# Kernel tuning notes

Hardware: AMD Instinct MI355X
Metric: run time of the kernel (lower is better)

Reference implementation:

```python
import jax, jax.numpy as jnp
import numpy as np

B, S, H, F, G = 8, 2048, 1024, 4096, 128
EPS = 1e-5


def setup_inputs() -> dict:
    key = jax.random.key(0)
    ks = jax.random.split(key, 8)
    x = jax.random.normal(ks[0], (B, S, H), dtype=jnp.float32)
    ln_gamma = jnp.ones((H,), jnp.float32)
    ln_beta = jnp.zeros((H,), jnp.float32)
    # int8-style quantized weights stored as int32 in [0, 256) with zero-point 128
    fc1_q = jax.random.randint(ks[1], (H, F), 0, 256, dtype=jnp.int32)
    fc2_q = jax.random.randint(ks[2], (F, H), 0, 256, dtype=jnp.int32)
    # per-group scales (one scale per 128 rows of K, per output column)
    fc1_scales = jax.random.uniform(ks[3], (H // G, F), jnp.float32) * 0.02 + 0.001
    fc2_scales = jax.random.uniform(ks[4], (F // G, H), jnp.float32) * 0.02 + 0.001
    fc1_bias = jax.random.normal(ks[5], (F,), jnp.float32) * 0.02
    fc2_bias = jax.random.normal(ks[6], (H,), jnp.float32) * 0.02
    return {"x": x, "ln_gamma": ln_gamma, "ln_beta": ln_beta,
            "fc1_q": fc1_q, "fc1_scales": fc1_scales, "fc1_bias": fc1_bias,
            "fc2_q": fc2_q, "fc2_scales": fc2_scales, "fc2_bias": fc2_bias}


def _dequant(q, scales, g):
    # q: [K, N] int, scales: [K//g, N]; zero-point 128 symmetric int8 scheme
    K, N = q.shape
    w = (q.astype(jnp.float32) - 128.0).reshape(K // g, g, N) * scales[:, None, :]
    return w.reshape(K, N)


def reference(x, ln_gamma, ln_beta, fc1_q, fc1_scales, fc1_bias, fc2_q, fc2_scales, fc2_bias):
    residual = x
    # LayerNorm over last dim
    mu = jnp.mean(x, axis=-1, keepdims=True)
    var = jnp.mean(jnp.square(x - mu), axis=-1, keepdims=True)
    h = (x - mu) * jax.lax.rsqrt(var + EPS) * ln_gamma + ln_beta
    hf = h.reshape(-1, H)                       # [B*S, H]
    w1 = _dequant(fc1_q, fc1_scales, G)         # [H, F]
    y = hf @ w1 + fc1_bias                      # [B*S, F]
    y = jax.nn.silu(y)                          # dropout is identity at inference
    w2 = _dequant(fc2_q, fc2_scales, G)         # [F, H]
    z = y @ w2 + fc2_bias                       # [B*S, H]
    return residual + 0.5 * z.reshape(residual.shape)
```

## Files before the change

kernel.cpp:

```cpp
#include <hip/hip_runtime.h>
#include <hip/hip_bf16.h>

#define HH 1024
#define FF 4096
#define MTOT (8 * 2048)

typedef __attribute__((ext_vector_type(4))) float f32x4;
typedef __attribute__((ext_vector_type(8))) short bf16x8;

__device__ inline void async_load16(const void* g, void* l) {
    __builtin_amdgcn_global_load_lds(
        (const __attribute__((address_space(1))) unsigned int*)g,
        (__attribute__((address_space(3))) unsigned int*)l, 16, 0, 0);
}
__device__ inline unsigned lds_off(void* p) {
    return (unsigned)(size_t)(__attribute__((address_space(3))) char*)p;
}
template<int OFF>
__device__ inline bf16x8 dsr(unsigned addr) {
    bf16x8 r;
    asm volatile("ds_read_b128 %0, %1 offset:%2" : "=v"(r) : "v"(addr), "n"(OFF));
    return r;
}
#define SBAR()  __builtin_amdgcn_s_barrier()
template<int N>
__device__ inline void LGKM() {
    asm volatile("s_waitcnt lgkmcnt(%0)" :: "n"(N));
    __builtin_amdgcn_sched_barrier(0);
}
#define WAIT_VM0() asm volatile("s_waitcnt vmcnt(0)")

template<int BUF, int MH>
__device__ inline void ldA(bf16x8 (&d)[4][2], unsigned vA0, unsigned vA1) {
    constexpr int B = BUF * 32768 + MH * 8192;
    d[0][0] = dsr<B + 0>(vA0);     d[0][1] = dsr<B + 0>(vA1);
    d[1][0] = dsr<B + 2048>(vA0);  d[1][1] = dsr<B + 2048>(vA1);
    d[2][0] = dsr<B + 4096>(vA0);  d[2][1] = dsr<B + 4096>(vA1);
    d[3][0] = dsr<B + 6144>(vA0);  d[3][1] = dsr<B + 6144>(vA1);
}
template<int BUF, int NH>
__device__ inline void ldB(bf16x8 (&d)[2][2], unsigned vB0, unsigned vB1) {
    constexpr int B = BUF * 32768 + NH * 4096;
    d[0][0] = dsr<B + 0>(vB0);     d[0][1] = dsr<B + 0>(vB1);
    d[1][0] = dsr<B + 2048>(vB0);  d[1][1] = dsr<B + 2048>(vB1);
}

__global__ void dequant_t_kernel(const int* __restrict__ q,
                                 const float* __restrict__ scales,
                                 __hip_bfloat16* __restrict__ wt,
                                 int K, int N)
{
    __shared__ float tile[32][33];
    const int n0 = blockIdx.x * 32, k0 = blockIdx.y * 32;
    const int tx = threadIdx.x, ty = threadIdx.y;
#pragma unroll
    for (int i = 0; i < 32; i += 8) {
        int k = k0 + ty + i, n = n0 + tx;
        float s = scales[(size_t)(k >> 7) * N + n];
        tile[ty + i][tx] = (float)(q[(size_t)k * N + n] - 128) * s;
    }
    __syncthreads();
#pragma unroll
    for (int i = 0; i < 32; i += 8) {
        int n = n0 + ty + i, k = k0 + tx;
        wt[(size_t)n * K + k] = __float2bfloat16(tile[tx][ty + i]);
    }
}

__global__ __launch_bounds__(256)
void ln_kernel(const float* __restrict__ x, const float* __restrict__ gamma,
               const float* __restrict__ beta, __hip_bfloat16* __restrict__ hf,
               int m0)
{
    const int row = m0 + blockIdx.x;
    const float4 v = ((const float4*)(x + (size_t)row * HH))[threadIdx.x];
    float s  = v.x + v.y + v.z + v.w;
    float ss = v.x * v.x + v.y * v.y + v.z * v.z + v.w * v.w;
#pragma unroll
    for (int o = 32; o > 0; o >>= 1) { s += __shfl_down(s, o); ss += __shfl_down(ss, o); }
    __shared__ float red[8];
    const int wid = threadIdx.x >> 6, lane = threadIdx.x & 63;
    if (lane == 0) { red[wid] = s; red[4 + wid] = ss; }
    __syncthreads();
    if (threadIdx.x == 0) {
        red[0] = red[0] + red[1] + red[2] + red[3];
        red[4] = red[4] + red[5] + red[6] + red[7];
    }
    __syncthreads();
    const float mu   = red[0] * (1.f / HH);
    const float rstd = rsqrtf(red[4] * (1.f / HH) - mu * mu + 1e-5f);
    const float4 g = ((const float4*)gamma)[threadIdx.x];
    const float4 b = ((const float4*)beta)[threadIdx.x];
    float h0 = (v.x - mu) * rstd * g.x + b.x;
    float h1 = (v.y - mu) * rstd * g.y + b.y;
    float h2 = (v.z - mu) * rstd * g.z + b.z;
    float h3 = (v.w - mu) * rstd * g.w + b.w;
    __hip_bfloat16 t0 = __float2bfloat16(h0), t1 = __float2bfloat16(h1);
    __hip_bfloat16 t2 = __float2bfloat16(h2), t3 = __float2bfloat16(h3);
    ushort4 o;
    o.x = *(unsigned short*)&t0; o.y = *(unsigned short*)&t1;
    o.z = *(unsigned short*)&t2; o.w = *(unsigned short*)&t3;
    ((ushort4*)(hf + (size_t)blockIdx.x * HH))[threadIdx.x] = o;
}

template<int EPI, int KK>
__global__ __launch_bounds__(512, 2)
void gemm256(const __hip_bfloat16* __restrict__ A,
             const __hip_bfloat16* __restrict__ Bt,
             const float* __restrict__ bias,
             const float* __restrict__ resid,
             void* __restrict__ outv,
             int N, int nbx)
{
    __shared__ __align__(16) short SM[65536];
    constexpr int NT = KK >> 6;

    const int nwg = (int)gridDim.x, b = (int)blockIdx.x;
    const int q = nwg >> 3, r = nwg & 7;
    const int xcd = b & 7, pos = b >> 3;
    const int bid = (xcd < r) ? xcd * (q + 1) + pos
                              : r * (q + 1) + (xcd - r) * q + pos;
    const int bx = bid % nbx, by = bid / nbx;
    const int rowA0 = by * 256, colB0 = bx * 256;

    const int tid = (int)threadIdx.x;
    const int lane = tid & 63, wid = tid >> 6;
    const int wr = wid >> 2, wc = wid & 3;
    const int lrow = lane & 15, kg = lane >> 4;
    const int swz = lrow & 7;

    const int srow = tid >> 3;
    const int sgs  = (tid & 7) ^ (srow & 7);
    const __hip_bfloat16* aSrc = A  + (size_t)(rowA0 + srow) * KK + sgs * 8;
    const __hip_bfloat16* bSrc = Bt + (size_t)(colB0 + srow) * KK + sgs * 8;
    short* aDst = SM + srow * 64 + (tid & 7) * 8;
    short* bDst = SM + 32768 + srow * 64 + (tid & 7) * 8;

    const unsigned asB = lds_off(SM);
    const unsigned k0off = (unsigned)((kg ^ swz) << 4);
    const unsigned k1off = (unsigned)(((4 + kg) ^ swz) << 4);
    const unsigned vA0 = asB + (unsigned)((wr * 128 + lrow) * 128) + k0off;
    const unsigned vA1 = asB + (unsigned)((wr * 128 + lrow) * 128) + k1off;
    const unsigned vB0 = asB + 65536u + (unsigned)((wc * 64 + lrow) * 128) + k0off;
    const unsigned vB1 = asB + 65536u + (unsigned)((wc * 64 + lrow) * 128) + k1off;

    auto stA = [&](int buf, int t, int half) {
        const size_t ko = (size_t)t * 64;
        short* d = aDst + buf * 16384 + half * 8192;
        const __hip_bfloat16* s0 = aSrc + (size_t)(half * 128) * KK + ko;
        async_load16(s0, d);
        async_load16(s0 + (size_t)64 * KK, d + 4096);
    };
    auto stB = [&](int buf, int t, int half) {
        const size_t ko = (size_t)t * 64;
        short* d = bDst + buf * 16384 + half * 8192;
        const __hip_bfloat16* s0 = bSrc + (size_t)(half * 128) * KK + ko;
        async_load16(s0, d);
        async_load16(s0 + (size_t)64 * KK, d + 4096);
    };

    f32x4 acc[8][4] = {};
    auto mf = [&](const bf16x8 (&a)[4][2], const bf16x8 (&bb)[2][2], int mh, int nh) {
        __builtin_amdgcn_s_setprio(1);
#pragma unroll
        for (int ks = 0; ks < 2; ++ks)
#pragma unroll
            for (int m2 = 0; m2 < 4; ++m2)
#pragma unroll
                for (int n2 = 0; n2 < 2; ++n2)
                    acc[mh * 4 + m2][nh * 2 + n2] =
                        __builtin_amdgcn_mfma_f32_16x16x32_bf16(
                            a[m2][ks], bb[n2][ks], acc[mh * 4 + m2][nh * 2 + n2], 0, 0, 0);
        __builtin_amdgcn_s_setprio(0);
    };

    stA(0, 0, 0); stA(0, 0, 1); stB(0, 0, 0); stB(0, 0, 1);
    WAIT_VM0();
    SBAR();

    bf16x8 a0[4][2], a1[4][2], b0[2][2], b1[2][2];
    const int NI = NT >> 1;
    for (int i = 0; i < NI; ++i) {
        const int c = 2 * i, n = 2 * i + 1;
        stA(1, n, 0); stA(1, n, 1); stB(1, n, 0); stB(1, n, 1);
        ldA<0, 0>(a0, vA0, vA1);
        ldB<0, 0>(b0, vB0, vB1);
        ldB<0, 1>(b1, vB0, vB1);
        ldA<0, 1>(a1, vA0, vA1);
        LGKM<12>();
        mf(a0, b0, 0, 0);
        LGKM<8>();
        mf(a0, b1, 0, 1);
        LGKM<0>();
        mf(a1, b0, 1, 0);
        mf(a1, b1, 1, 1);
        WAIT_VM0();
        SBAR();
        if (i < NI - 1) { stA(0, c + 2, 0); stA(0, c + 2, 1);
                          stB(0, c + 2, 0); stB(0, c + 2, 1); }
        ldA<1, 0>(a0, vA0, vA1);
        ldB<1, 0>(b0, vB0, vB1);
        ldB<1, 1>(b1, vB0, vB1);
        ldA<1, 1>(a1, vA0, vA1);
        LGKM<12>();
        mf(a0, b0, 0, 0);
        LGKM<8>();
        mf(a0, b1, 0, 1);
        LGKM<0>();
        mf(a1, b0, 1, 0);
        mf(a1, b1, 1, 1);
        WAIT_VM0();
        SBAR();
    }

    __syncthreads();

    if (EPI == 0) {
        short* smh = SM;
#pragma unroll
        for (int ni = 0; ni < 4; ++ni) {
            const int col = wc * 64 + ni * 16 + lrow;
            const float bv = bias[colB0 + col];
#pragma unroll
            for (int mi = 0; mi < 8; ++mi) {
#pragma unroll
                for (int j = 0; j < 4; ++j) {
                    const int rowl = wr * 128 + mi * 16 + kg * 4 + j;
                    const float v = acc[mi][ni][j] + bv;
                    const float sv = v / (1.f + __expf(-v));
                    const __hip_bfloat16 hb = __float2bfloat16(sv);
                    const int sidx = rowl * 256 + ((((col >> 3) ^ (rowl & 7)) << 3) | (col & 7));
                    smh[sidx] = *(const short*)&hb;
                }
            }
        }
        __syncthreads();
        __hip_bfloat16* yp = (__hip_bfloat16*)outv;
#pragma unroll
        for (int p = 0; p < 16; ++p) {
            const int idx = p * 512 + tid;
            const int rowl = idx >> 5, s = idx & 31;
            const bf16x8 v8 = *(const bf16x8*)&smh[rowl * 256 + ((s ^ (rowl & 7)) << 3)];
            *(bf16x8*)(yp + (size_t)(rowA0 + rowl) * N + colB0 + s * 8) = v8;
        }
    } else {
        float* smf = (float*)SM;
        float* op = (float*)outv;
#pragma unroll
        for (int h = 0; h < 2; ++h) {
            if (wr == h) {
#pragma unroll
                for (int ni = 0; ni < 4; ++ni) {
                    const int col = wc * 64 + ni * 16 + lrow;
                    const float bv = bias[colB0 + col];
#pragma unroll
                    for (int mi = 0; mi < 8; ++mi) {
#pragma unroll
                        for (int j = 0; j < 4; ++j) {
                            const int rowl = mi * 16 + kg * 4 + j;
                            const float v = acc[mi][ni][j] + bv;
                            const int fidx = rowl * 256 +
                                ((((col >> 2) ^ (rowl & 7)) << 2) | (col & 3));
                            smf[fidx] = v;
                        }
                    }
                }
            }
            __syncthreads();
#pragma unroll
            for (int p = 0; p < 16; ++p) {
                const int idx = p * 512 + tid;
                const int rowl = idx >> 6, s = idx & 63;
                const f32x4 v4 = *(const f32x4*)&smf[rowl * 256 + ((s ^ (rowl & 7)) << 2)];
                const size_t g = (size_t)(rowA0 + h * 128 + rowl) * N + colB0 + s * 4;
                const float4 rv = *(const float4*)&resid[g];
                float4 o4;
                o4.x = rv.x + 0.5f * v4[0];
                o4.y = rv.y + 0.5f * v4[1];
                o4.z = rv.z + 0.5f * v4[2];
                o4.w = rv.w + 0.5f * v4[3];
                *(float4*)&op[g] = o4;
            }
            __syncthreads();
        }
    }
}

extern "C" void kernel_launch(void* const* d_in, const int* in_sizes, int n_in,
                              void* d_out, int out_size, void* d_ws, size_t ws_size,
                              hipStream_t stream)
{
    const float* x      = (const float*)d_in[0];
    const float* gamma  = (const float*)d_in[1];
    const float* beta   = (const float*)d_in[2];
    const int*   fc1_q  = (const int*)d_in[3];
    const float* fc1_s  = (const float*)d_in[4];
    const float* fc1_b  = (const float*)d_in[5];
    const int*   fc2_q  = (const int*)d_in[6];
    const float* fc2_s  = (const float*)d_in[7];
    const float* fc2_b  = (const float*)d_in[8];
    float* out = (float*)d_out;

    char* ws = (char*)d_ws;
    __hip_bfloat16* w1t = (__hip_bfloat16*)ws;
    __hip_bfloat16* w2t = (__hip_bfloat16*)(ws + (size_t)FF * HH * 2);
    char* dyn = ws + (size_t)2 * FF * HH * 2;
    const size_t avail = ws_size - (size_t)2 * FF * HH * 2;

    int MC = (int)(avail / ((size_t)(HH + FF) * 2));
    MC = (MC / 256) * 256;
    if (MC > MTOT) MC = MTOT;
    if (MC < 256)  MC = 256;

    __hip_bfloat16* hf_c = (__hip_bfloat16*)dyn;
    __hip_bfloat16* y_c  = (__hip_bfloat16*)(dyn + (size_t)MC * HH * 2);

    dequant_t_kernel<<<dim3(FF / 32, HH / 32), dim3(32, 8), 0, stream>>>(
        fc1_q, fc1_s, w1t, HH, FF);
    dequant_t_kernel<<<dim3(HH / 32, FF / 32), dim3(32, 8), 0, stream>>>(
        fc2_q, fc2_s, w2t, FF, HH);

    for (int m0 = 0; m0 < MTOT; m0 += MC) {
        const int mc = (MTOT - m0 < MC) ? (MTOT - m0) : MC;
        ln_kernel<<<mc, 256, 0, stream>>>(x, gamma, beta, hf_c, m0);
        gemm256<0, HH><<<dim3((FF / 256) * (mc / 256)), 512, 0, stream>>>(
            hf_c, w1t, fc1_b, nullptr, (void*)y_c, FF, FF / 256);
        gemm256<1, FF><<<dim3((HH / 256) * (mc / 256)), 512, 0, stream>>>(
            y_c, w2t, fc2_b, x + (size_t)m0 * HH, (void*)(out + (size_t)m0 * HH),
            HH, HH / 256);
    }
}
```

Before: 313.9 us.

## Switch both FFN GEMMs to int8 MFMA with dynamic activation quantization

Weights are repacked to transposed int8 without dequantizing. LayerNorm output is quantized per row to int8, and the SiLU output is quantized to int8 with one scale per row per 128-column block. Both GEMMs use i8 MFMA and apply the per-group weight scales and activation scales in fp32 after every 128-wide K chunk. The intent is to double matrix-core throughput and halve operand traffic compared with bf16. The cost is extra VALU rescaling per chunk, less overlap between LDS reads and MFMA, and lower numerical accuracy from quantizing activations.

```diff
diff --git a/kernel.cpp b/kernel.cpp
--- a/kernel.cpp
+++ b/kernel.cpp
@@ -6,6 +6,7 @@
 #define MTOT (8 * 2048)
 
 typedef __attribute__((ext_vector_type(4))) float f32x4;
+typedef __attribute__((ext_vector_type(4))) int   i32x4;
 typedef __attribute__((ext_vector_type(8))) short bf16x8;
 
 __device__ inline void async_load16(const void* g, void* l) {
@@ -17,60 +18,60 @@
     return (unsigned)(size_t)(__attribute__((address_space(3))) char*)p;
 }
 template<int OFF>
-__device__ inline bf16x8 dsr(unsigned addr) {
-    bf16x8 r;
+__device__ inline i32x4 dsr(unsigned addr) {
+    i32x4 r;
     asm volatile("ds_read_b128 %0, %1 offset:%2" : "=v"(r) : "v"(addr), "n"(OFF));
     return r;
 }
 #define SBAR()  __builtin_amdgcn_s_barrier()
-template<int N>
-__device__ inline void LGKM() {
-    asm volatile("s_waitcnt lgkmcnt(%0)" :: "n"(N));
-    __builtin_amdgcn_sched_barrier(0);
-}
+#define LGKM0() do { asm volatile("s_waitcnt lgkmcnt(0)"); \
+                     __builtin_amdgcn_sched_barrier(0); } while (0)
 #define WAIT_VM0() asm volatile("s_waitcnt vmcnt(0)")
 
-template<int BUF, int MH>
-__device__ inline void ldA(bf16x8 (&d)[4][2], unsigned vA0, unsigned vA1) {
-    constexpr int B = BUF * 32768 + MH * 8192;
-    d[0][0] = dsr<B + 0>(vA0);     d[0][1] = dsr<B + 0>(vA1);
-    d[1][0] = dsr<B + 2048>(vA0);  d[1][1] = dsr<B + 2048>(vA1);
-    d[2][0] = dsr<B + 4096>(vA0);  d[2][1] = dsr<B + 4096>(vA1);
-    d[3][0] = dsr<B + 6144>(vA0);  d[3][1] = dsr<B + 6144>(vA1);
-}
-template<int BUF, int NH>
-__device__ inline void ldB(bf16x8 (&d)[2][2], unsigned vB0, unsigned vB1) {
-    constexpr int B = BUF * 32768 + NH * 4096;
-    d[0][0] = dsr<B + 0>(vB0);     d[0][1] = dsr<B + 0>(vB1);
-    d[1][0] = dsr<B + 2048>(vB0);  d[1][1] = dsr<B + 2048>(vB1);
-}
-
-__global__ void dequant_t_kernel(const int* __restrict__ q,
-                                 const float* __restrict__ scales,
-                                 __hip_bfloat16* __restrict__ wt,
-                                 int K, int N)
+__device__ inline float b2f(short s) {
+    unsigned u = ((unsigned)(unsigned short)s) << 16;
+    float f; __builtin_memcpy(&f, &u, 4); return f;
+}
+__device__ inline int q8(float f) {
+    int v = __float2int_rn(f);
+    return v < -127 ? -127 : (v > 127 ? 127 : v);
+}
+
+template<int B0, int MH>
+__device__ inline void ldA8(i32x4 (&d)[4][2], unsigned v0, unsigned v1) {
+    constexpr int B = B0 + MH * 8192;
+    d[0][0] = dsr<B + 0>(v0);     d[0][1] = dsr<B + 0>(v1);
+    d[1][0] = dsr<B + 2048>(v0);  d[1][1] = dsr<B + 2048>(v1);
+    d[2][0] = dsr<B + 4096>(v0);  d[2][1] = dsr<B + 4096>(v1);
+    d[3][0] = dsr<B + 6144>(v0);  d[3][1] = dsr<B + 6144>(v1);
+}
+template<int B0>
+__device__ inline void ldB8(i32x4 (&d)[4][2], unsigned v0, unsigned v1) {
+    d[0][0] = dsr<B0 + 0>(v0);     d[0][1] = dsr<B0 + 0>(v1);
+    d[1][0] = dsr<B0 + 2048>(v0);  d[1][1] = dsr<B0 + 2048>(v1);
+    d[2][0] = dsr<B0 + 4096>(v0);  d[2][1] = dsr<B0 + 4096>(v1);
+    d[3][0] = dsr<B0 + 6144>(v0);  d[3][1] = dsr<B0 + 6144>(v1);
+}
+
+__global__ void repack_kernel(const int* __restrict__ q, char* __restrict__ wq,
+                              int K, int N)
 {
-    __shared__ float tile[32][33];
+    __shared__ char tile[32][33];
     const int n0 = blockIdx.x * 32, k0 = blockIdx.y * 32;
     const int tx = threadIdx.x, ty = threadIdx.y;
 #pragma unroll
-    for (int i = 0; i < 32; i += 8) {
-        int k = k0 + ty + i, n = n0 + tx;
-        float s = scales[(size_t)(k >> 7) * N + n];
-        tile[ty + i][tx] = (float)(q[(size_t)k * N + n] - 128) * s;
-    }
-    __syncthreads();
-#pragma unroll
-    for (int i = 0; i < 32; i += 8) {
-        int n = n0 + ty + i, k = k0 + tx;
-        wt[(size_t)n * K + k] = __float2bfloat16(tile[tx][ty + i]);
-    }
+    for (int i = 0; i < 32; i += 8)
+        tile[ty + i][tx] = (char)(q[(size_t)(k0 + ty + i) * N + n0 + tx] - 128);
+    __syncthreads();
+#pragma unroll
+    for (int i = 0; i < 32; i += 8)
+        wq[(size_t)(n0 + ty + i) * K + k0 + tx] = tile[tx][ty + i];
 }
 
 __global__ __launch_bounds__(256)
-void ln_kernel(const float* __restrict__ x, const float* __restrict__ gamma,
-               const float* __restrict__ beta, __hip_bfloat16* __restrict__ hf,
-               int m0)
+void ln_q_kernel(const float* __restrict__ x, const float* __restrict__ gamma,
+                 const float* __restrict__ beta, char* __restrict__ hq,
+                 float* __restrict__ hs, int m0)
 {
     const int row = m0 + blockIdx.x;
     const float4 v = ((const float4*)(x + (size_t)row * HH))[threadIdx.x];
@@ -95,29 +96,37 @@
     float h1 = (v.y - mu) * rstd * g.y + b.y;
     float h2 = (v.z - mu) * rstd * g.z + b.z;
     float h3 = (v.w - mu) * rstd * g.w + b.w;
-    __hip_bfloat16 t0 = __float2bfloat16(h0), t1 = __float2bfloat16(h1);
-    __hip_bfloat16 t2 = __float2bfloat16(h2), t3 = __float2bfloat16(h3);
-    ushort4 o;
-    o.x = *(unsigned short*)&t0; o.y = *(unsigned short*)&t1;
-    o.z = *(unsigned short*)&t2; o.w = *(unsigned short*)&t3;
-    ((ushort4*)(hf + (size_t)blockIdx.x * HH))[threadIdx.x] = o;
-}
-
-template<int EPI, int KK>
+    float mx = fmaxf(fmaxf(fabsf(h0), fabsf(h1)), fmaxf(fabsf(h2), fabsf(h3)));
+#pragma unroll
+    for (int o = 32; o > 0; o >>= 1) mx = fmaxf(mx, __shfl_down(mx, o));
+    __syncthreads();
+    if (lane == 0) red[wid] = mx;
+    __syncthreads();
+    if (threadIdx.x == 0)
+        red[0] = fmaxf(fmaxf(red[0], red[1]), fmaxf(red[2], red[3]));
+    __syncthreads();
+    const float m = fmaxf(red[0], 1e-12f);
+    const float inv = 127.f / m;
+    const int q0 = q8(h0 * inv), q1 = q8(h1 * inv), q2 = q8(h2 * inv), q3 = q8(h3 * inv);
+    ((int*)(hq + (size_t)blockIdx.x * HH))[threadIdx.x] =
+        (q0 & 255) | ((q1 & 255) << 8) | ((q2 & 255) << 16) | ((q3 & 255) << 24);
+    if (threadIdx.x == 0) hs[blockIdx.x] = m / 127.f;
+}
+
 __global__ __launch_bounds__(512, 2)
-void gemm256(const __hip_bfloat16* __restrict__ A,
-             const __hip_bfloat16* __restrict__ Bt,
-             const float* __restrict__ bias,
-             const float* __restrict__ resid,
-             void* __restrict__ outv,
-             int N, int nbx)
+void gemm1_i8(const char* __restrict__ A, const char* __restrict__ Bt,
+              const float* __restrict__ s1, const float* __restrict__ hs,
+              const float* __restrict__ bias,
+              char* __restrict__ yq, float* __restrict__ ys,
+              int Mrows, int nbx)
 {
-    __shared__ __align__(16) short SM[65536];
-    constexpr int NT = KK >> 6;
-
-    const int nwg = (int)gridDim.x, b = (int)blockIdx.x;
+    constexpr int KK = HH;
+    constexpr int NT = KK / 128;
+    __shared__ __align__(16) char SMc[131072];
+
+    const int nwg = (int)gridDim.x, bq = (int)blockIdx.x;
     const int q = nwg >> 3, r = nwg & 7;
-    const int xcd = b & 7, pos = b >> 3;
+    const int xcd = bq & 7, pos = bq >> 3;
     const int bid = (xcd < r) ? xcd * (q + 1) + pos
                               : r * (q + 1) + (xcd - r) * q + pos;
     const int bx = bid % nbx, by = bid / nbx;
@@ -131,12 +140,12 @@
 
     const int srow = tid >> 3;
     const int sgs  = (tid & 7) ^ (srow & 7);
-    const __hip_bfloat16* aSrc = A  + (size_t)(rowA0 + srow) * KK + sgs * 8;
-    const __hip_bfloat16* bSrc = Bt + (size_t)(colB0 + srow) * KK + sgs * 8;
-    short* aDst = SM + srow * 64 + (tid & 7) * 8;
-    short* bDst = SM + 32768 + srow * 64 + (tid & 7) * 8;
-
-    const unsigned asB = lds_off(SM);
+    const char* aSrc = A  + (size_t)(rowA0 + srow) * KK + sgs * 16;
+    const char* bSrc = Bt + (size_t)(colB0 + srow) * KK + sgs * 16;
+    char* aDst = SMc + srow * 128 + (tid & 7) * 16;
+    char* bDst = SMc + 65536 + srow * 128 + (tid & 7) * 16;
+
+    const unsigned asB = lds_off(SMc);
     const unsigned k0off = (unsigned)((kg ^ swz) << 4);
     const unsigned k1off = (unsigned)(((4 + kg) ^ swz) << 4);
     const unsigned vA0 = asB + (unsigned)((wr * 128 + lrow) * 128) + k0off;
@@ -144,145 +153,298 @@
     const unsigned vB0 = asB + 65536u + (unsigned)((wc * 64 + lrow) * 128) + k0off;
     const unsigned vB1 = asB + 65536u + (unsigned)((wc * 64 + lrow) * 128) + k1off;
 
-    auto stA = [&](int buf, int t, int half) {
-        const size_t ko = (size_t)t * 64;
-        short* d = aDst + buf * 16384 + half * 8192;
-        const __hip_bfloat16* s0 = aSrc + (size_t)(half * 128) * KK + ko;
+    auto stA = [&](int buf, int t) {
+        const char* s0 = aSrc + t * 128;
+        char* d = aDst + buf * 32768;
         async_load16(s0, d);
-        async_load16(s0 + (size_t)64 * KK, d + 4096);
-    };
-    auto stB = [&](int buf, int t, int half) {
-        const size_t ko = (size_t)t * 64;
-        short* d = bDst + buf * 16384 + half * 8192;
-        const __hip_bfloat16* s0 = bSrc + (size_t)(half * 128) * KK + ko;
+        async_load16(s0 + (size_t)64 * KK,  d + 8192);
+        async_load16(s0 + (size_t)128 * KK, d + 16384);
+        async_load16(s0 + (size_t)192 * KK, d + 24576);
+    };
+    auto stB = [&](int buf, int t) {
+        const char* s0 = bSrc + t * 128;
+        char* d = bDst + buf * 32768;
         async_load16(s0, d);
-        async_load16(s0 + (size_t)64 * KK, d + 4096);
+        async_load16(s0 + (size_t)64 * KK,  d + 8192);
+        async_load16(s0 + (size_t)128 * KK, d + 16384);
+        async_load16(s0 + (size_t)192 * KK, d + 24576);
     };
 
     f32x4 acc[8][4] = {};
-    auto mf = [&](const bf16x8 (&a)[4][2], const bf16x8 (&bb)[2][2], int mh, int nh) {
+    const i32x4 zero = {0, 0, 0, 0};
+    i32x4 a[4][2], b[4][2];
+    float sc[4];
+
+    auto half = [&](int mh) {
         __builtin_amdgcn_s_setprio(1);
 #pragma unroll
-        for (int ks = 0; ks < 2; ++ks)
-#pragma unroll
-            for (int m2 = 0; m2 < 4; ++m2)
-#pragma unroll
-                for (int n2 = 0; n2 < 2; ++n2)
-                    acc[mh * 4 + m2][nh * 2 + n2] =
-                        __builtin_amdgcn_mfma_f32_16x16x32_bf16(
-                            a[m2][ks], bb[n2][ks], acc[mh * 4 + m2][nh * 2 + n2], 0, 0, 0);
+        for (int mi = 0; mi < 4; ++mi)
+#pragma unroll
+            for (int ni = 0; ni < 4; ++ni) {
+                i32x4 t = __builtin_amdgcn_mfma_i32_16x16x64_i8(a[mi][0], b[ni][0], zero, 0, 0, 0);
+                t = __builtin_amdgcn_mfma_i32_16x16x64_i8(a[mi][1], b[ni][1], t, 0, 0, 0);
+                f32x4& A_ = acc[mh * 4 + mi][ni];
+                A_[0] += sc[ni] * (float)t[0];
+                A_[1] += sc[ni] * (float)t[1];
+                A_[2] += sc[ni] * (float)t[2];
+                A_[3] += sc[ni] * (float)t[3];
+            }
         __builtin_amdgcn_s_setprio(0);
     };
 
-    stA(0, 0, 0); stA(0, 0, 1); stB(0, 0, 0); stB(0, 0, 1);
+    stA(0, 0); stB(0, 0);
     WAIT_VM0();
     SBAR();
 
-    bf16x8 a0[4][2], a1[4][2], b0[2][2], b1[2][2];
     const int NI = NT >> 1;
     for (int i = 0; i < NI; ++i) {
         const int c = 2 * i, n = 2 * i + 1;
-        stA(1, n, 0); stA(1, n, 1); stB(1, n, 0); stB(1, n, 1);
-        ldA<0, 0>(a0, vA0, vA1);
-        ldB<0, 0>(b0, vB0, vB1);
-        ldB<0, 1>(b1, vB0, vB1);
-        ldA<0, 1>(a1, vA0, vA1);
-        LGKM<12>();
-        mf(a0, b0, 0, 0);
-        LGKM<8>();
-        mf(a0, b1, 0, 1);
-        LGKM<0>();
-        mf(a1, b0, 1, 0);
-        mf(a1, b1, 1, 1);
+#pragma unroll
+        for (int ni = 0; ni < 4; ++ni)
+            sc[ni] = s1[(size_t)c * FF + colB0 + wc * 64 + ni * 16 + lrow];
+        stA(1, n); stB(1, n);
+        ldB8<0>(b, vB0, vB1);
+        ldA8<0, 0>(a, vA0, vA1);
+        LGKM0();
+        half(0);
+        ldA8<0, 1>(a, vA0, vA1);
+        LGKM0();
+        half(1);
         WAIT_VM0();
         SBAR();
-        if (i < NI - 1) { stA(0, c + 2, 0); stA(0, c + 2, 1);
-                          stB(0, c + 2, 0); stB(0, c + 2, 1); }
-        ldA<1, 0>(a0, vA0, vA1);
-        ldB<1, 0>(b0, vB0, vB1);
-        ldB<1, 1>(b1, vB0, vB1);
-        ldA<1, 1>(a1, vA0, vA1);
-        LGKM<12>();
-        mf(a0, b0, 0, 0);
-        LGKM<8>();
-        mf(a0, b1, 0, 1);
-        LGKM<0>();
-        mf(a1, b0, 1, 0);
-        mf(a1, b1, 1, 1);
+#pragma unroll
+        for (int ni = 0; ni < 4; ++ni)
+            sc[ni] = s1[(size_t)n * FF + colB0 + wc * 64 + ni * 16 + lrow];
+        if (i < NI - 1) { stA(0, c + 2); stB(0, c + 2); }
+        ldB8<32768>(b, vB0, vB1);
+        ldA8<32768, 0>(a, vA0, vA1);
+        LGKM0();
+        half(0);
+        ldA8<32768, 1>(a, vA0, vA1);
+        LGKM0();
+        half(1);
         WAIT_VM0();
         SBAR();
     }
 
     __syncthreads();
-
-    if (EPI == 0) {
-        short* smh = SM;
-#pragma unroll
-        for (int ni = 0; ni < 4; ++ni) {
-            const int col = wc * 64 + ni * 16 + lrow;
-            const float bv = bias[colB0 + col];
-#pragma unroll
-            for (int mi = 0; mi < 8; ++mi) {
-#pragma unroll
-                for (int j = 0; j < 4; ++j) {
-                    const int rowl = wr * 128 + mi * 16 + kg * 4 + j;
-                    const float v = acc[mi][ni][j] + bv;
-                    const float sv = v / (1.f + __expf(-v));
-                    const __hip_bfloat16 hb = __float2bfloat16(sv);
-                    const int sidx = rowl * 256 + ((((col >> 3) ^ (rowl & 7)) << 3) | (col & 7));
-                    smh[sidx] = *(const short*)&hb;
+    short* smh = (short*)SMc;
+    f32x4 hv[8];
+#pragma unroll
+    for (int mi = 0; mi < 8; ++mi)
+        hv[mi] = *(const f32x4*)(hs + rowA0 + wr * 128 + mi * 16 + kg * 4);
+#pragma unroll
+    for (int ni = 0; ni < 4; ++ni) {
+        const int col = wc * 64 + ni * 16 + lrow;
+        const float bv = bias[colB0 + col];
+#pragma unroll
+        for (int mi = 0; mi < 8; ++mi) {
+#pragma unroll
+            for (int j = 0; j < 4; ++j) {
+                const int rowl = wr * 128 + mi * 16 + kg * 4 + j;
+                const float v = hv[mi][j] * acc[mi][ni][j] + bv;
+                const float sv = v / (1.f + __expf(-v));
+                const __hip_bfloat16 hb = __float2bfloat16(sv);
+                smh[rowl * 256 + ((((col >> 3) ^ (rowl & 7)) << 3) | (col & 7))] =
+                    *(const short*)&hb;
+            }
+        }
+    }
+    __syncthreads();
+    {
+        const int rowl = tid >> 1, hf2 = tid & 1;
+        const int r7 = rowl & 7;
+        short* rp = smh + rowl * 256;
+        float mx = 0.f;
+#pragma unroll
+        for (int u = 0; u < 16; ++u) {
+            const int sslot = hf2 * 16 + u;
+            const bf16x8 vv = *(const bf16x8*)(rp + ((sslot ^ r7) << 3));
+#pragma unroll
+            for (int e = 0; e < 8; ++e) mx = fmaxf(mx, fabsf(b2f(vv[e])));
+        }
+        const float mc = fmaxf(mx, 1e-12f);
+        const float ysv = mc / 127.f, inv = 127.f / mc;
+        ys[(size_t)(bx * 2 + hf2) * Mrows + rowA0 + rowl] = ysv;
+        char* yrow = yq + (size_t)(rowA0 + rowl) * FF + colB0 + hf2 * 128;
+#pragma unroll
+        for (int u2 = 0; u2 < 8; ++u2) {
+            const int s0 = hf2 * 16 + u2 * 2, s1_ = s0 + 1;
+            const bf16x8 v0 = *(const bf16x8*)(rp + ((s0 ^ r7) << 3));
+            const bf16x8 v1 = *(const bf16x8*)(rp + ((s1_ ^ r7) << 3));
+            int w[4];
+#pragma unroll
+            for (int k = 0; k < 2; ++k) {
+                const bf16x8& vv = k ? v1 : v0;
+#pragma unroll
+                for (int hq4 = 0; hq4 < 2; ++hq4) {
+                    const int e0 = hq4 * 4;
+                    const int a0 = q8(b2f(vv[e0 + 0]) * inv), a1 = q8(b2f(vv[e0 + 1]) * inv);
+                    const int a2 = q8(b2f(vv[e0 + 2]) * inv), a3 = q8(b2f(vv[e0 + 3]) * inv);
+                    w[k * 2 + hq4] = (a0 & 255) | ((a1 & 255) << 8) |
+                                     ((a2 & 255) << 16) | ((a3 & 255) << 24);
+                }
+            }
+            *(i32x4*)(yrow + u2 * 16) = (i32x4){w[0], w[1], w[2], w[3]};
+        }
+    }
+}
+
+__global__ __launch_bounds__(512, 2)
+void gemm2_i8(const char* __restrict__ A, const char* __restrict__ Bt,
+              const float* __restrict__ s2, const float* __restrict__ ys,
+              const float* __restrict__ bias, const float* __restrict__ resid,
+              float* __restrict__ out, int Mrows, int nbx)
+{
+    constexpr int KK = FF;
+    constexpr int NT = KK / 128;
+    __shared__ __align__(16) char SMc[131072];
+
+    const int nwg = (int)gridDim.x, bq = (int)blockIdx.x;
+    const int q = nwg >> 3, r = nwg & 7;
+    const int xcd = bq & 7, pos = bq >> 3;
+    const int bid = (xcd < r) ? xcd * (q + 1) + pos
+                              : r * (q + 1) + (xcd - r) * q + pos;
+    const int bx = bid % nbx, by = bid / nbx;
+    const int rowA0 = by * 256, colB0 = bx * 256;
+
+    const int tid = (int)threadIdx.x;
+    const int lane = tid & 63, wid = tid >> 6;
+    const int wr = wid >> 2, wc = wid & 3;
+    const int lrow = lane & 15, kg = lane >> 4;
+    const int swz = lrow & 7;
+
+    const int srow = tid >> 3;
+    const int sgs  = (tid & 7) ^ (srow & 7);
+    const char* aSrc = A  + (size_t)(rowA0 + srow) * KK + sgs * 16;
+    const char* bSrc = Bt + (size_t)(colB0 + srow) * KK + sgs * 16;
+    char* aDst = SMc + srow * 128 + (tid & 7) * 16;
+    char* bDst = SMc + 65536 + srow * 128 + (tid & 7) * 16;
+
+    const unsigned asB = lds_off(SMc);
+    const unsigned k0off = (unsigned)((kg ^ swz) << 4);
+    const unsigned k1off = (unsigned)(((4 + kg) ^ swz) << 4);
+    const unsigned vA0 = asB + (unsigned)((wr * 128 + lrow) * 128) + k0off;
+    const unsigned vA1 = asB + (unsigned)((wr * 128 + lrow) * 128) + k1off;
+    const unsigned vB0 = asB + 65536u + (unsigned)((wc * 64 + lrow) * 128) + k0off;
+    const unsigned vB1 = asB + 65536u + (unsigned)((wc * 64 + lrow) * 128) + k1off;
+
+    auto stA = [&](int buf, int t) {
+        const char* s0 = aSrc + t * 128;
+        char* d = aDst + buf * 32768;
+        async_load16(s0, d);
+        async_load16(s0 + (size_t)64 * KK,  d + 8192);
+        async_load16(s0 + (size_t)128 * KK, d + 16384);
+        async_load16(s0 + (size_t)192 * KK, d + 24576);
+    };
+    auto stB = [&](int buf, int t) {
+        const char* s0 = bSrc + t * 128;
+        char* d = bDst + buf * 32768;
+        async_load16(s0, d);
+        async_load16(s0 + (size_t)64 * KK,  d + 8192);
+        async_load16(s0 + (size_t)128 * KK, d + 16384);
+        async_load16(s0 + (size_t)192 * KK, d + 24576);
+    };
+
+    f32x4 acc[8][4] = {};
+    const i32x4 zero = {0, 0, 0, 0};
+    i32x4 a[4][2], b[4][2];
+    f32x4 yv[8];
+    float sc[4];
+
+    auto half = [&](int mh) {
+        __builtin_amdgcn_s_setprio(1);
+#pragma unroll
+        for (int mi = 0; mi < 4; ++mi)
+#pragma unroll
+            for (int ni = 0; ni < 4; ++ni) {
+                i32x4 t = __builtin_amdgcn_mfma_i32_16x16x64_i8(a[mi][0], b[ni][0], zero, 0, 0, 0);
+                t = __builtin_amdgcn_mfma_i32_16x16x64_i8(a[mi][1], b[ni][1], t, 0, 0, 0);
+                f32x4& A_ = acc[mh * 4 + mi][ni];
+                const f32x4& yw = yv[mh * 4 + mi];
+                A_[0] += yw[0] * sc[ni] * (float)t[0];
+                A_[1] += yw[1] * sc[ni] * (float)t[1];
+                A_[2] += yw[2] * sc[ni] * (float)t[2];
+                A_[3] += yw[3] * sc[ni] * (float)t[3];
+            }
+        __builtin_amdgcn_s_setprio(0);
+    };
+    auto loadScales = [&](int g) {
+#pragma unroll
+        for (int mi = 0; mi < 8; ++mi)
+            yv[mi] = *(const f32x4*)(ys + (size_t)g * Mrows + rowA0 + wr * 128 + mi * 16 + kg * 4);
+#pragma unroll
+        for (int ni = 0; ni < 4; ++ni)
+            sc[ni] = s2[(size_t)g * HH + colB0 + wc * 64 + ni * 16 + lrow];
+    };
+
+    stA(0, 0); stB(0, 0);
+    WAIT_VM0();
+    SBAR();
+
+    const int NI = NT >> 1;
+    for (int i = 0; i < NI; ++i) {
+        const int c = 2 * i, n = 2 * i + 1;
+        loadScales(c);
+        stA(1, n); stB(1, n);
+        ldB8<0>(b, vB0, vB1);
+        ldA8<0, 0>(a, vA0, vA1);
+        LGKM0();
+        half(0);
+        ldA8<0, 1>(a, vA0, vA1);
+        LGKM0();
+        half(1);
+        WAIT_VM0();
+        SBAR();
+        loadScales(n);
+        if (i < NI - 1) { stA(0, c + 2); stB(0, c + 2); }
+        ldB8<32768>(b, vB0, vB1);
+        ldA8<32768, 0>(a, vA0, vA1);
+        LGKM0();
+        half(0);
+        ldA8<32768, 1>(a, vA0, vA1);
+        LGKM0();
+        half(1);
+        WAIT_VM0();
+        SBAR();
+    }
+
+    __syncthreads();
+    float* smf = (float*)SMc;
+#pragma unroll
+    for (int h = 0; h < 2; ++h) {
+        if (wr == h) {
+#pragma unroll
+            for (int ni = 0; ni < 4; ++ni) {
+                const int col = wc * 64 + ni * 16 + lrow;
+                const float bv = bias[colB0 + col];
+#pragma unroll
+                for (int mi = 0; mi < 8; ++mi) {
+#pragma unroll
+                    for (int j = 0; j < 4; ++j) {
+                        const int rowl = mi * 16 + kg * 4 + j;
+                        const float v = acc[mi][ni][j] + bv;
+                        smf[rowl * 256 + ((((col >> 2) ^ (rowl & 7)) << 2) | (col & 3))] = v;
+                    }
                 }
             }
         }
         __syncthreads();
-        __hip_bfloat16* yp = (__hip_bfloat16*)outv;
 #pragma unroll
         for (int p = 0; p < 16; ++p) {
             const int idx = p * 512 + tid;
-            const int rowl = idx >> 5, s = idx & 31;
-            const bf16x8 v8 = *(const bf16x8*)&smh[rowl * 256 + ((s ^ (rowl & 7)) << 3)];
-            *(bf16x8*)(yp + (size_t)(rowA0 + rowl) * N + colB0 + s * 8) = v8;
+            const int rowl = idx >> 6, s = idx & 63;
+            const f32x4 v4 = *(const f32x4*)&smf[rowl * 256 + ((s ^ (rowl & 7)) << 2)];
+            const size_t g = (size_t)(rowA0 + h * 128 + rowl) * HH + colB0 + s * 4;
+            const float4 rv = *(const float4*)&resid[g];
+            float4 o4;
+            o4.x = rv.x + 0.5f * v4[0];
+            o4.y = rv.y + 0.5f * v4[1];
+            o4.z = rv.z + 0.5f * v4[2];
+            o4.w = rv.w + 0.5f * v4[3];
+            *(float4*)&out[g] = o4;
         }
-    } else {
-        float* smf = (float*)SM;
-        float* op = (float*)outv;
-#pragma unroll
-        for (int h = 0; h < 2; ++h) {
-            if (wr == h) {
-#pragma unroll
-                for (int ni = 0; ni < 4; ++ni) {
-                    const int col = wc * 64 + ni * 16 + lrow;
-                    const float bv = bias[colB0 + col];
-#pragma unroll
-                    for (int mi = 0; mi < 8; ++mi) {
-#pragma unroll
-                        for (int j = 0; j < 4; ++j) {
-                            const int rowl = mi * 16 + kg * 4 + j;
-                            const float v = acc[mi][ni][j] + bv;
-                            const int fidx = rowl * 256 +
-                                ((((col >> 2) ^ (rowl & 7)) << 2) | (col & 3));
-                            smf[fidx] = v;
-                        }
-                    }
-                }
-            }
-            __syncthreads();
-#pragma unroll
-            for (int p = 0; p < 16; ++p) {
-                const int idx = p * 512 + tid;
-                const int rowl = idx >> 6, s = idx & 63;
-                const f32x4 v4 = *(const f32x4*)&smf[rowl * 256 + ((s ^ (rowl & 7)) << 2)];
-                const size_t g = (size_t)(rowA0 + h * 128 + rowl) * N + colB0 + s * 4;
-                const float4 rv = *(const float4*)&resid[g];
-                float4 o4;
-                o4.x = rv.x + 0.5f * v4[0];
-                o4.y = rv.y + 0.5f * v4[1];
-                o4.z = rv.z + 0.5f * v4[2];
-                o4.w = rv.w + 0.5f * v4[3];
-                *(float4*)&op[g] = o4;
-            }
-            __syncthreads();
-        }
+        __syncthreads();
     }
 }
 
@@ -302,31 +464,32 @@
     float* out = (float*)d_out;
 
     char* ws = (char*)d_ws;
-    __hip_bfloat16* w1t = (__hip_bfloat16*)ws;
-    __hip_bfloat16* w2t = (__hip_bfloat16*)(ws + (size_t)FF * HH * 2);
-    char* dyn = ws + (size_t)2 * FF * HH * 2;
-    const size_t avail = ws_size - (size_t)2 * FF * HH * 2;
-
-    int MC = (int)(avail / ((size_t)(HH + FF) * 2));
+    char* w1q = ws;
+    char* w2q = ws + (size_t)FF * HH;
+    char* base = ws + (size_t)2 * FF * HH;
+    const size_t avail = ws_size - (size_t)2 * FF * HH;
+
+    const size_t per_row = HH + FF + 4 + 128;
+    int MC = (int)(avail / per_row);
     MC = (MC / 256) * 256;
     if (MC > MTOT) MC = MTOT;
     if (MC < 256)  MC = 256;
 
-    __hip_bfloat16* hf_c = (__hip_bfloat16*)dyn;
-    __hip_bfloat16* y_c  = (__hip_bfloat16*)(dyn + (size_t)MC * HH * 2);
-
-    dequant_t_kernel<<<dim3(FF / 32, HH / 32), dim3(32, 8), 0, stream>>>(
-        fc1_q, fc1_s, w1t, HH, FF);
-    dequant_t_kernel<<<dim3(HH / 32, FF / 32), dim3(32, 8), 0, stream>>>(
-        fc2_q, fc2_s, w2t, FF, HH);
+    float* hs = (float*)base;
+    float* ys = (float*)(base + (size_t)MC * 4);
+    char*  hq = base + (size_t)MC * 4 + (size_t)32 * MC * 4;
+    char*  yq = hq + (size_t)MC * HH;
+
+    repack_kernel<<<dim3(FF / 32, HH / 32), dim3(32, 8), 0, stream>>>(fc1_q, w1q, HH, FF);
+    repack_kernel<<<dim3(HH / 32, FF / 32), dim3(32, 8), 0, stream>>>(fc2_q, w2q, FF, HH);
 
     for (int m0 = 0; m0 < MTOT; m0 += MC) {
         const int mc = (MTOT - m0 < MC) ? (MTOT - m0) : MC;
-        ln_kernel<<<mc, 256, 0, stream>>>(x, gamma, beta, hf_c, m0);
-        gemm256<0, HH><<<dim3((FF / 256) * (mc / 256)), 512, 0, stream>>>(
-            hf_c, w1t, fc1_b, nullptr, (void*)y_c, FF, FF / 256);
-        gemm256<1, FF><<<dim3((HH / 256) * (mc / 256)), 512, 0, stream>>>(
-            y_c, w2t, fc2_b, x + (size_t)m0 * HH, (void*)(out + (size_t)m0 * HH),
-            HH, HH / 256);
-    }
-}
+        ln_q_kernel<<<mc, 256, 0, stream>>>(x, gamma, beta, hq, hs, m0);
+        gemm1_i8<<<dim3((FF / 256) * (mc / 256)), 512, 0, stream>>>(
+            hq, w1q, fc1_s, hs, fc1_b, yq, ys, mc, FF / 256);
+        gemm2_i8<<<dim3((HH / 256) * (mc / 256)), 512, 0, stream>>>(
+            yq, w2q, fc2_s, ys, fc2_b, x + (size_t)m0 * HH, out + (size_t)m0 * HH,
+            mc, HH / 256);
+    }
+}
```

Result: slower. 783.0 us (+149.4%).

## Shrink GEMM block tile from 256x256 to 128x128 with 256 threads

Applied to the files above, without the earlier changes.

Replaces the 256x256-tile, 512-thread GEMM with a 128x128-tile, 256-thread version using half the LDS, a 4x4 accumulator per wave and one full lgkmcnt wait before all MFMAs. The aim is more blocks and possibly higher occupancy. In exchange, each block reuses its loaded data less, so global and L2 traffic rise. The staggered LDS-read/MFMA overlap is also dropped. The epilogues are adapted to the smaller tile, and the FC2 epilogue no longer needs its two-pass split.

```diff
diff --git a/kernel.cpp b/kernel.cpp
--- a/kernel.cpp
+++ b/kernel.cpp
@@ -23,26 +23,17 @@
     return r;
 }
 #define SBAR()  __builtin_amdgcn_s_barrier()
-template<int N>
-__device__ inline void LGKM() {
-    asm volatile("s_waitcnt lgkmcnt(%0)" :: "n"(N));
-    __builtin_amdgcn_sched_barrier(0);
-}
+#define LGKM0() do { asm volatile("s_waitcnt lgkmcnt(0)"); \
+                     __builtin_amdgcn_sched_barrier(0); } while (0)
 #define WAIT_VM0() asm volatile("s_waitcnt vmcnt(0)")
 
-template<int BUF, int MH>
-__device__ inline void ldA(bf16x8 (&d)[4][2], unsigned vA0, unsigned vA1) {
-    constexpr int B = BUF * 32768 + MH * 8192;
-    d[0][0] = dsr<B + 0>(vA0);     d[0][1] = dsr<B + 0>(vA1);
-    d[1][0] = dsr<B + 2048>(vA0);  d[1][1] = dsr<B + 2048>(vA1);
-    d[2][0] = dsr<B + 4096>(vA0);  d[2][1] = dsr<B + 4096>(vA1);
-    d[3][0] = dsr<B + 6144>(vA0);  d[3][1] = dsr<B + 6144>(vA1);
-}
-template<int BUF, int NH>
-__device__ inline void ldB(bf16x8 (&d)[2][2], unsigned vB0, unsigned vB1) {
-    constexpr int B = BUF * 32768 + NH * 4096;
-    d[0][0] = dsr<B + 0>(vB0);     d[0][1] = dsr<B + 0>(vB1);
-    d[1][0] = dsr<B + 2048>(vB0);  d[1][1] = dsr<B + 2048>(vB1);
+template<int BUF>
+__device__ inline void ldF(bf16x8 (&d)[4][2], unsigned v0, unsigned v1) {
+    constexpr int B = BUF * 16384;
+    d[0][0] = dsr<B + 0>(v0);     d[0][1] = dsr<B + 0>(v1);
+    d[1][0] = dsr<B + 2048>(v0);  d[1][1] = dsr<B + 2048>(v1);
+    d[2][0] = dsr<B + 4096>(v0);  d[2][1] = dsr<B + 4096>(v1);
+    d[3][0] = dsr<B + 6144>(v0);  d[3][1] = dsr<B + 6144>(v1);
 }
 
 __global__ void dequant_t_kernel(const int* __restrict__ q,
@@ -104,15 +95,15 @@
 }
 
 template<int EPI, int KK>
-__global__ __launch_bounds__(512, 2)
-void gemm256(const __hip_bfloat16* __restrict__ A,
+__global__ __launch_bounds__(256, 2)
+void gemm128(const __hip_bfloat16* __restrict__ A,
              const __hip_bfloat16* __restrict__ Bt,
              const float* __restrict__ bias,
              const float* __restrict__ resid,
              void* __restrict__ outv,
              int N, int nbx)
 {
-    __shared__ __align__(16) short SM[65536];
+    __shared__ __align__(16) short SM[32768];
     constexpr int NT = KK >> 6;
 
     const int nwg = (int)gridDim.x, b = (int)blockIdx.x;
@@ -121,11 +112,11 @@
     const int bid = (xcd < r) ? xcd * (q + 1) + pos
                               : r * (q + 1) + (xcd - r) * q + pos;
     const int bx = bid % nbx, by = bid / nbx;
-    const int rowA0 = by * 256, colB0 = bx * 256;
+    const int rowA0 = by * 128, colB0 = bx * 128;
 
     const int tid = (int)threadIdx.x;
     const int lane = tid & 63, wid = tid >> 6;
-    const int wr = wid >> 2, wc = wid & 3;
+    const int wr = wid >> 1, wc = wid & 1;
     const int lrow = lane & 15, kg = lane >> 4;
     const int swz = lrow & 7;
 
@@ -134,87 +125,72 @@
     const __hip_bfloat16* aSrc = A  + (size_t)(rowA0 + srow) * KK + sgs * 8;
     const __hip_bfloat16* bSrc = Bt + (size_t)(colB0 + srow) * KK + sgs * 8;
     short* aDst = SM + srow * 64 + (tid & 7) * 8;
-    short* bDst = SM + 32768 + srow * 64 + (tid & 7) * 8;
+    short* bDst = SM + 16384 + srow * 64 + (tid & 7) * 8;
 
     const unsigned asB = lds_off(SM);
     const unsigned k0off = (unsigned)((kg ^ swz) << 4);
     const unsigned k1off = (unsigned)(((4 + kg) ^ swz) << 4);
-    const unsigned vA0 = asB + (unsigned)((wr * 128 + lrow) * 128) + k0off;
-    const unsigned vA1 = asB + (unsigned)((wr * 128 + lrow) * 128) + k1off;
-    const unsigned vB0 = asB + 65536u + (unsigned)((wc * 64 + lrow) * 128) + k0off;
-    const unsigned vB1 = asB + 65536u + (unsigned)((wc * 64 + lrow) * 128) + k1off;
-
-    auto stA = [&](int buf, int t, int half) {
-        const size_t ko = (size_t)t * 64;
-        short* d = aDst + buf * 16384 + half * 8192;
-        const __hip_bfloat16* s0 = aSrc + (size_t)(half * 128) * KK + ko;
-        async_load16(s0, d);
-        async_load16(s0 + (size_t)64 * KK, d + 4096);
+    const unsigned vA0 = asB + (unsigned)((wr * 64 + lrow) * 128) + k0off;
+    const unsigned vA1 = asB + (unsigned)((wr * 64 + lrow) * 128) + k1off;
+    const unsigned vB0 = asB + 32768u + (unsigned)((wc * 64 + lrow) * 128) + k0off;
+    const unsigned vB1 = asB + 32768u + (unsigned)((wc * 64 + lrow) * 128) + k1off;
+
+    auto stA = [&](int buf, int t) {
+        const __hip_bfloat16* s0 = aSrc + (size_t)t * 64;
+        short* d = aDst + buf * 8192;
+        async_load16(s0,                    d);
+        async_load16(s0 + (size_t)32 * KK,  d + 2048);
+        async_load16(s0 + (size_t)64 * KK,  d + 4096);
+        async_load16(s0 + (size_t)96 * KK,  d + 6144);
     };
-    auto stB = [&](int buf, int t, int half) {
-        const size_t ko = (size_t)t * 64;
-        short* d = bDst + buf * 16384 + half * 8192;
-        const __hip_bfloat16* s0 = bSrc + (size_t)(half * 128) * KK + ko;
-        async_load16(s0, d);
-        async_load16(s0 + (size_t)64 * KK, d + 4096);
+    auto stB = [&](int buf, int t) {
+        const __hip_bfloat16* s0 = bSrc + (size_t)t * 64;
+        short* d = bDst + buf * 8192;
+        async_load16(s0,                    d);
+        async_load16(s0 + (size_t)32 * KK,  d + 2048);
+        async_load16(s0 + (size_t)64 * KK,  d + 4096);
+        async_load16(s0 + (size_t)96 * KK,  d + 6144);
     };
 
-    f32x4 acc[8][4] = {};
-    auto mf = [&](const bf16x8 (&a)[4][2], const bf16x8 (&bb)[2][2], int mh, int nh) {
+    f32x4 acc[4][4] = {};
+    bf16x8 a[4][2], bb[4][2];
+    auto mfall = [&]() {
         __builtin_amdgcn_s_setprio(1);
 #pragma unroll
         for (int ks = 0; ks < 2; ++ks)
 #pragma unroll
-            for (int m2 = 0; m2 < 4; ++m2)
-#pragma unroll
-                for (int n2 = 0; n2 < 2; ++n2)
-                    acc[mh * 4 + m2][nh * 2 + n2] =
-                        __builtin_amdgcn_mfma_f32_16x16x32_bf16(
-                            a[m2][ks], bb[n2][ks], acc[mh * 4 + m2][nh * 2 + n2], 0, 0, 0);
+            for (int mi = 0; mi < 4; ++mi)
+#pragma unroll
+                for (int ni = 0; ni < 4; ++ni)
+                    acc[mi][ni] = __builtin_amdgcn_mfma_f32_16x16x32_bf16(
+                        a[mi][ks], bb[ni][ks], acc[mi][ni], 0, 0, 0);
         __builtin_amdgcn_s_setprio(0);
     };
 
-    stA(0, 0, 0); stA(0, 0, 1); stB(0, 0, 0); stB(0, 0, 1);
+    stA(0, 0); stB(0, 0);
     WAIT_VM0();
     SBAR();
 
-    bf16x8 a0[4][2], a1[4][2], b0[2][2], b1[2][2];
     const int NI = NT >> 1;
     for (int i = 0; i < NI; ++i) {
         const int c = 2 * i, n = 2 * i + 1;
-        stA(1, n, 0); stA(1, n, 1); stB(1, n, 0); stB(1, n, 1);
-        ldA<0, 0>(a0, vA0, vA1);
-        ldB<0, 0>(b0, vB0, vB1);
-        ldB<0, 1>(b1, vB0, vB1);
-        ldA<0, 1>(a1, vA0, vA1);
-        LGKM<12>();
-        mf(a0, b0, 0, 0);
-        LGKM<8>();
-        mf(a0, b1, 0, 1);
-        LGKM<0>();
-        mf(a1, b0, 1, 0);
-        mf(a1, b1, 1, 1);
+        stA(1, n); stB(1, n);
+        ldF<0>(bb, vB0, vB1);
+        ldF<0>(a, vA0, vA1);
+        LGKM0();
+        mfall();
         WAIT_VM0();
         SBAR();
-        if (i < NI - 1) { stA(0, c + 2, 0); stA(0, c + 2, 1);
-                          stB(0, c + 2, 0); stB(0, c + 2, 1); }
-        ldA<1, 0>(a0, vA0, vA1);
-        ldB<1, 0>(b0, vB0, vB1);
-        ldB<1, 1>(b1, vB0, vB1);
-        ldA<1, 1>(a1, vA0, vA1);
-        LGKM<12>();
-        mf(a0, b0, 0, 0);
-        LGKM<8>();
-        mf(a0, b1, 0, 1);
-        LGKM<0>();
-        mf(a1, b0, 1, 0);
-        mf(a1, b1, 1, 1);
+        if (i < NI - 1) { stA(0, c + 2); stB(0, c + 2); }
+        ldF<1>(bb, vB0, vB1);
+        ldF<1>(a, vA0, vA1);
+        LGKM0();
+        mfall();
         WAIT_VM0();
         SBAR();
     }
 
     __syncthreads();
-
     if (EPI == 0) {
         short* smh = SM;
 #pragma unroll
@@ -222,66 +198,58 @@
             const int col = wc * 64 + ni * 16 + lrow;
             const float bv = bias[colB0 + col];
 #pragma unroll
-            for (int mi = 0; mi < 8; ++mi) {
+            for (int mi = 0; mi < 4; ++mi) {
 #pragma unroll
                 for (int j = 0; j < 4; ++j) {
-                    const int rowl = wr * 128 + mi * 16 + kg * 4 + j;
+                    const int rowl = wr * 64 + mi * 16 + kg * 4 + j;
                     const float v = acc[mi][ni][j] + bv;
                     const float sv = v / (1.f + __expf(-v));
                     const __hip_bfloat16 hb = __float2bfloat16(sv);
-                    const int sidx = rowl * 256 + ((((col >> 3) ^ (rowl & 7)) << 3) | (col & 7));
-                    smh[sidx] = *(const short*)&hb;
+                    smh[rowl * 128 + ((((col >> 3) ^ (rowl & 7)) << 3) | (col & 7))] =
+                        *(const short*)&hb;
                 }
             }
         }
         __syncthreads();
         __hip_bfloat16* yp = (__hip_bfloat16*)outv;
 #pragma unroll
-        for (int p = 0; p < 16; ++p) {
-            const int idx = p * 512 + tid;
-            const int rowl = idx >> 5, s = idx & 31;
-            const bf16x8 v8 = *(const bf16x8*)&smh[rowl * 256 + ((s ^ (rowl & 7)) << 3)];
+        for (int p = 0; p < 8; ++p) {
+            const int idx = p * 256 + tid;
+            const int rowl = idx >> 4, s = idx & 15;
+            const bf16x8 v8 = *(const bf16x8*)&smh[rowl * 128 + ((s ^ (rowl & 7)) << 3)];
             *(bf16x8*)(yp + (size_t)(rowA0 + rowl) * N + colB0 + s * 8) = v8;
         }
     } else {
         float* smf = (float*)SM;
         float* op = (float*)outv;
 #pragma unroll
-        for (int h = 0; h < 2; ++h) {
-            if (wr == h) {
-#pragma unroll
-                for (int ni = 0; ni < 4; ++ni) {
-                    const int col = wc * 64 + ni * 16 + lrow;
-                    const float bv = bias[colB0 + col];
-#pragma unroll
-                    for (int mi = 0; mi < 8; ++mi) {
-#pragma unroll
-                        for (int j = 0; j < 4; ++j) {
-                            const int rowl = mi * 16 + kg * 4 + j;
-                            const float v = acc[mi][ni][j] + bv;
-                            const int fidx = rowl * 256 +
-                                ((((col >> 2) ^ (rowl & 7)) << 2) | (col & 3));
-                            smf[fidx] = v;
-                        }
-                    }
+        for (int ni = 0; ni < 4; ++ni) {
+            const int col = wc * 64 + ni * 16 + lrow;
+            const float bv = bias[colB0 + col];
+#pragma unroll
+            for (int mi = 0; mi < 4; ++mi) {
+#pragma unroll
+                for (int j = 0; j < 4; ++j) {
+                    const int rowl = wr * 64 + mi * 16 + kg * 4 + j;
+                    const float v = acc[mi][ni][j] + bv;
+                    smf[rowl * 128 + ((((col >> 2) ^ (rowl & 7)) << 2) | (col & 3))] = v;
                 }
             }
-            __syncthreads();
-#pragma unroll
-            for (int p = 0; p < 16; ++p) {
-                const int idx = p * 512 + tid;
-                const int rowl = idx >> 6, s = idx & 63;
-                const f32x4 v4 = *(const f32x4*)&smf[rowl * 256 + ((s ^ (rowl & 7)) << 2)];
-                const size_t g = (size_t)(rowA0 + h * 128 + rowl) * N + colB0 + s * 4;
-                const float4 rv = *(const float4*)&resid[g];
-                float4 o4;
-                o4.x = rv.x + 0.5f * v4[0];
-                o4.y = rv.y + 0.5f * v4[1];
-                o4.z = rv.z + 0.5f * v4[2];
-                o4.w = rv.w + 0.5f * v4[3];
-                *(float4*)&op[g] = o4;
-            }
-            __syncthreads();
+        }
+        __syncthreads();
+#pragma unroll
+        for (int p = 0; p < 16; ++p) {
+            const int idx = p * 256 + tid;
+            const int rowl = idx >> 5, s = idx & 31;
+            const f32x4 v4 = *(const f32x4*)&smf[rowl * 128 + ((s ^ (rowl & 7)) << 2)];
+            const size_t g = (size_t)(rowA0 + rowl) * N + colB0 + s * 4;
+            const float4 rv = *(const float4*)&resid[g];
+            float4 o4;
+            o4.x = rv.x + 0.5f * v4[0];
+            o4.y = rv.y + 0.5f * v4[1];
+            o4.z = rv.z + 0.5f * v4[2];
+            o4.w = rv.w + 0.5f * v4[3];
+            *(float4*)&op[g] = o4;
         }
     }
 }
@@ -323,10 +291,10 @@
     for (int m0 = 0; m0 < MTOT; m0 += MC) {
         const int mc = (MTOT - m0 < MC) ? (MTOT - m0) : MC;
         ln_kernel<<<mc, 256, 0, stream>>>(x, gamma, beta, hf_c, m0);
-        gemm256<0, HH><<<dim3((FF / 256) * (mc / 256)), 512, 0, stream>>>(
-            hf_c, w1t, fc1_b, nullptr, (void*)y_c, FF, FF / 256);
-        gemm256<1, FF><<<dim3((HH / 256) * (mc / 256)), 512, 0, stream>>>(
+        gemm128<0, HH><<<dim3((FF / 128) * (mc / 128)), 256, 0, stream>>>(
+            hf_c, w1t, fc1_b, nullptr, (void*)y_c, FF, FF / 128);
+        gemm128<1, FF><<<dim3((HH / 128) * (mc / 128)), 256, 0, stream>>>(
             y_c, w2t, fc2_b, x + (size_t)m0 * HH, (void*)(out + (size_t)m0 * HH),
-            HH, HH / 256);
-    }
-}
+            HH, HH / 128);
+    }
+}
```

Result: slower. 337.2 us (+7.4%).
